# Kernel optimization log

Measured on AMD Instinct MI355X. Metric: run time of the kernel, lower is better.

Reference implementation:

```python
import jax, jax.numpy as jnp
import numpy as np

DIM = 1024
HEADS = 16
HEAD_DIM = DIM // HEADS


def setup_inputs() -> dict:
    key = jax.random.key(0)
    ks = jax.random.split(key, 12)
    B, Tq, Tk = 2, 2048, 2048
    inp = {
        "query": jax.random.normal(ks[0], (B, Tq, DIM), jnp.float32),
        "key": jax.random.normal(ks[1], (B, Tk, DIM), jnp.float32),
        "value": jax.random.normal(ks[2], (B, Tk, DIM), jnp.float32),
        "mask": jax.random.randint(ks[3], (B, 1, Tq, Tk), 0, 2, jnp.int32),
        # xavier-uniform projection weights (stored [out,in] like torch), zero biases
        "wq": jax.random.uniform(ks[4], (DIM, DIM), jnp.float32, -1.0, 1.0) * np.sqrt(6.0 / (2 * DIM)),
        "wk": jax.random.uniform(ks[5], (DIM, DIM), jnp.float32, -1.0, 1.0) * np.sqrt(6.0 / (2 * DIM)),
        "wv": jax.random.uniform(ks[6], (DIM, DIM), jnp.float32, -1.0, 1.0) * np.sqrt(6.0 / (2 * DIM)),
        "wo": jax.random.uniform(ks[7], (DIM, DIM), jnp.float32, -1.0, 1.0) * np.sqrt(6.0 / (2 * DIM)),
        "bq": jnp.zeros((DIM,), jnp.float32),
        "bk": jnp.zeros((DIM,), jnp.float32),
        "bv": jnp.zeros((DIM,), jnp.float32),
        "bo": jnp.zeros((DIM,), jnp.float32),
    }
    return inp


def reference(query, key, value, mask, wq, wk, wv, wo, bq, bk, bv, bo):
    B, Tq, C = query.shape
    Tk = key.shape[1]
    scale = 1.0 / np.sqrt(HEAD_DIM)
    # projections (torch Linear: x @ W.T + b) -> [B, H, T, Dh]
    q = (query @ wq.T + bq).reshape(B, Tq, HEADS, HEAD_DIM).transpose(0, 2, 1, 3)
    k = (key @ wk.T + bk).reshape(B, Tk, HEADS, HEAD_DIM).transpose(0, 2, 1, 3)
    v = (value @ wv.T + bv).reshape(B, Tk, HEADS, HEAD_DIM).transpose(0, 2, 1, 3)
    scores = jnp.einsum("bhqd,bhkd->bhqk", q, k) * scale
    scores = jnp.clip(scores, -100.0, 100.0)
    scores = jnp.where(mask == 0, -jnp.inf, scores)
    attn = jax.nn.softmax(scores, axis=-1)  # dropout is identity in eval
    out = jnp.einsum("bhqk,bhkd->bhqd", attn, v)
    out = out.transpose(0, 2, 1, 3).reshape(B, Tq, HEADS * HEAD_DIM)
    return out @ wo.T + bo
```

## Files before the change

### kernel.cpp

```cpp
#include <hip/hip_runtime.h>
#include <hip/hip_bf16.h>
#include <stdint.h>


typedef __bf16 bf16;
typedef __bf16 bf16x4 __attribute__((ext_vector_type(4)));
typedef __bf16 bf16x8 __attribute__((ext_vector_type(8)));
typedef float f32x4 __attribute__((ext_vector_type(4)));

#define MFMA_BF16(a, b, c) __builtin_amdgcn_mfma_f32_16x16x32_bf16((a), (b), (c), 0, 0, 0)
#define NEG_INF (-__builtin_inff())

__device__ __forceinline__ void async_load16(const void* g, void* l) {
  __builtin_amdgcn_global_load_lds((const __attribute__((address_space(1))) void*)g,
                                   (__attribute__((address_space(3))) void*)l, 16, 0, 0);
}

__global__ __launch_bounds__(256) void cvt_f32_bf16(
    const float* __restrict__ s0, const float* __restrict__ s1, const float* __restrict__ s2,
    const float* __restrict__ s3, const float* __restrict__ s4, const float* __restrict__ s5,
    const float* __restrict__ s6,
    bf16* __restrict__ d0, bf16* __restrict__ d1, bf16* __restrict__ d2,
    bf16* __restrict__ d3, bf16* __restrict__ d4, bf16* __restrict__ d5,
    bf16* __restrict__ d6) {
  const int z = blockIdx.y;
  const float* s = (z == 0) ? s0 : (z == 1) ? s1 : (z == 2) ? s2 : (z == 3) ? s3
                   : (z == 4) ? s4 : (z == 5) ? s5 : s6;
  bf16* d = (z == 0) ? d0 : (z == 1) ? d1 : (z == 2) ? d2 : (z == 3) ? d3
            : (z == 4) ? d4 : (z == 5) ? d5 : d6;
  const int n4 = (z < 3) ? (4 * 1024 * 1024 / 4) : (1024 * 1024 / 4);
  const int stride = gridDim.x * 256;
  for (int i = blockIdx.x * 256 + threadIdx.x; i < n4; i += stride) {
    const float4 v = ((const float4*)s)[i];
    bf16x4 o;
    o[0] = (bf16)v.x; o[1] = (bf16)v.y; o[2] = (bf16)v.z; o[3] = (bf16)v.w;
    ((bf16x4*)d)[i] = o;
  }
}

__global__ __launch_bounds__(256) void pack_mask_kernel(const int* __restrict__ mask,
                                                        unsigned long long* __restrict__ bits) {
  const int t = blockIdx.x * 256 + threadIdx.x;
  const int v = mask[t];
  const unsigned long long b = __ballot(v != 0);
  if ((threadIdx.x & 63) == 0) bits[t >> 6] = b;
}

__global__ __launch_bounds__(256) void gemm_bt_bias(
    const bf16* __restrict__ X0, const bf16* __restrict__ X1, const bf16* __restrict__ X2,
    const bf16* __restrict__ W0, const bf16* __restrict__ W1, const bf16* __restrict__ W2,
    const float* __restrict__ Bi0, const float* __restrict__ Bi1, const float* __restrict__ Bi2,
    bf16* __restrict__ O0, bf16* __restrict__ O1, bf16* __restrict__ O2,
    float* __restrict__ OF, int K, int N, int vz, int f32out) {
  const int z = blockIdx.z;
  const bf16* X   = (z == 0) ? X0  : (z == 1) ? X1  : X2;
  const bf16* W   = (z == 0) ? W0  : (z == 1) ? W1  : W2;
  const float* Bi = (z == 0) ? Bi0 : (z == 1) ? Bi1 : Bi2;
  bf16* O         = (z == 0) ? O0  : (z == 1) ? O1  : O2;

  __shared__ __align__(16) unsigned char smem_raw[34816];
  bf16* As  = (bf16*)smem_raw;
  bf16* Bs  = As + 128 * 64;
  bf16* Tt  = (bf16*)smem_raw;
  float* Tf = (float*)smem_raw;

  const int tid = threadIdx.x;
  const int lane = tid & 63;
  const int w = tid >> 6;
  const int la = lane & 15;
  const int qa = lane >> 4;
  const int m0 = blockIdx.x * 128;
  const int n0 = blockIdx.y * 128;
  const int wm = (w & 1) * 64;
  const int wn = (w >> 1) * 64;

  f32x4 acc[4][4];
  for (int i = 0; i < 4; ++i)
    for (int j = 0; j < 4; ++j) acc[i][j] = (f32x4){0.f, 0.f, 0.f, 0.f};

  for (int k0 = 0; k0 < K; k0 += 64) {
    for (int i = 0; i < 4; ++i) {
      const int cb = i * 256 + w * 64;
      const int c = cb + lane;
      const int row = c >> 3;
      const int cc = (c & 7) * 8;
      async_load16(X + (size_t)(m0 + row) * K + k0 + cc, As + (size_t)cb * 8);
      async_load16(W + (size_t)(n0 + row) * K + k0 + cc, Bs + (size_t)cb * 8);
    }
    __syncthreads();
    for (int kk = 0; kk < 64; kk += 32) {
      bf16x8 af[4], bfr[4];
      for (int mt = 0; mt < 4; ++mt)
        af[mt] = *(const bf16x8*)&As[(wm + mt * 16 + la) * 64 + kk + qa * 8];
      for (int nt = 0; nt < 4; ++nt)
        bfr[nt] = *(const bf16x8*)&Bs[(wn + nt * 16 + la) * 64 + kk + qa * 8];
      for (int mt = 0; mt < 4; ++mt)
        for (int nt = 0; nt < 4; ++nt)
          acc[mt][nt] = MFMA_BF16(af[mt], bfr[nt], acc[mt][nt]);
    }
    __syncthreads();
  }

  if (f32out) {
    for (int pass = 0; pass < 2; ++pass) {
      if ((w & 1) == pass) {
        for (int mt = 0; mt < 4; ++mt)
          for (int nt = 0; nt < 4; ++nt)
            for (int r = 0; r < 4; ++r) {
              const int rl = mt * 16 + qa * 4 + r;
              const int cl = wn + nt * 16 + la;
              Tf[rl * 132 + cl] = acc[mt][nt][r] + Bi[n0 + cl];
            }
      }
      __syncthreads();
      for (int i = 0; i < 8; ++i) {
        const int rl = i * 8 + (tid >> 5);
        const int cl = (tid & 31) * 4;
        const float4 vv = *(const float4*)&Tf[rl * 132 + cl];
        *(float4*)&OF[(size_t)(m0 + pass * 64 + rl) * N + n0 + cl] = vv;
      }
      __syncthreads();
    }
  } else if (z != vz) {
    for (int mt = 0; mt < 4; ++mt)
      for (int nt = 0; nt < 4; ++nt)
        for (int r = 0; r < 4; ++r) {
          const int rl = wm + mt * 16 + qa * 4 + r;
          const int cl = wn + nt * 16 + la;
          Tt[rl * 136 + cl] = (bf16)(acc[mt][nt][r] + Bi[n0 + cl]);
        }
    __syncthreads();
    for (int i = 0; i < 8; ++i) {
      const int rl = i * 16 + (tid >> 4);
      const int cc = (tid & 15) * 8;
      *(bf16x8*)&O[(size_t)(m0 + rl) * N + n0 + cc] = *(const bf16x8*)&Tt[rl * 136 + cc];
    }
  } else {
    for (int mt = 0; mt < 4; ++mt)
      for (int nt = 0; nt < 4; ++nt)
        for (int r = 0; r < 4; ++r) {
          const int rl = wm + mt * 16 + qa * 4 + r;
          const int cl = wn + nt * 16 + la;
          Tt[cl * 136 + rl] = (bf16)(acc[mt][nt][r] + Bi[n0 + cl]);
        }
    __syncthreads();
    const int bb = m0 >> 11;
    const int k0t = m0 & 2047;
    for (int i = 0; i < 8; ++i) {
      const int cl = i * 16 + (tid >> 4);
      const int rr = (tid & 15) * 8;
      *(bf16x8*)&O[((size_t)(bb * 1024 + n0 + cl)) * 2048 + k0t + rr] =
          *(const bf16x8*)&Tt[cl * 136 + rr];
    }
  }
}

__global__ __launch_bounds__(256, 3) void attn_kernel(
    const bf16* __restrict__ Qp, const bf16* __restrict__ Kp, const bf16* __restrict__ Vt,
    const unsigned long long* __restrict__ mbits, bf16* __restrict__ AO) {
  __shared__ bf16 Kb[2][64 * 64];
  __shared__ bf16 Vb[2][64 * 64];

  const int tid = threadIdx.x;
  const int lane = tid & 63;
  const int w = tid >> 6;
  const int la = lane & 15;
  const int qa = lane >> 4;
  const int la7 = la & 7;
  const int b = blockIdx.y >> 4;
  const int h = blockIdx.y & 15;
  const int q0 = blockIdx.x * 64 + w * 16;

  const float SCALE = 0.18033688011112042f;

  const size_t kbase = (size_t)(b * 2048) * 1024 + h * 64;
  const size_t vbase = ((size_t)(b * 16 + h) * 64) * 2048;
  const unsigned long long* mrow = mbits + ((size_t)(b * 2048 + q0 + la)) * 32;

  const int cb0 = w * 64;
  const int cb1 = 256 + w * 64;
  const int c0 = cb0 + lane, c1 = cb1 + lane;
  const int r0 = c0 >> 3, j0 = (c0 & 7) ^ (r0 & 7);
  const int r1 = c1 >> 3, j1 = (c1 & 7) ^ (r1 & 7);
  const bf16* kp0 = Kp + kbase + (size_t)r0 * 1024 + j0 * 8;
  const bf16* kp1 = Kp + kbase + (size_t)r1 * 1024 + j1 * 8;
  const bf16* vp0 = Vt + vbase + (size_t)r0 * 2048 + j0 * 8;
  const bf16* vp1 = Vt + vbase + (size_t)r1 * 2048 + j1 * 8;

  bf16x8 qf[2];
  for (int kk = 0; kk < 2; ++kk)
    qf[kk] = *(const bf16x8*)&Qp[(size_t)(b * 2048 + q0 + la) * 1024 + h * 64 + kk * 32 + qa * 8];

  bf16x8 ones;
  for (int j = 0; j < 8; ++j) ones[j] = (bf16)1.0f;

  f32x4 oacc[5];
  for (int d = 0; d < 5; ++d) oacc[d] = (f32x4){0.f, 0.f, 0.f, 0.f};

  async_load16(kp0, &Kb[0][cb0 * 8]);
  async_load16(kp1, &Kb[0][cb1 * 8]);
  async_load16(vp0, &Vb[0][cb0 * 8]);
  async_load16(vp1, &Vb[0][cb1 * 8]);
  __syncthreads();

  const int srcA = ((qa & 1) << 5) + la;
  const int srcB = srcA + 16;
  const bool hi = (qa >= 2);

  for (int kt = 0; kt < 32; ++kt) {
    const int p = kt & 1;
    const bf16* Kc = Kb[p];
    const bf16* Vc = Vb[p];

    if (kt < 31) {
      bf16* Kn = Kb[p ^ 1];
      bf16* Vn = Vb[p ^ 1];
      kp0 += 64 * 1024; kp1 += 64 * 1024;
      vp0 += 64;        vp1 += 64;
      async_load16(kp0, &Kn[cb0 * 8]);
      async_load16(kp1, &Kn[cb1 * 8]);
      async_load16(vp0, &Vn[cb0 * 8]);
      async_load16(vp1, &Vn[cb1 * 8]);
    }

    const unsigned long long mv = mrow[kt];

    f32x4 s[4];
    for (int nt = 0; nt < 4; ++nt) s[nt] = (f32x4){0.f, 0.f, 0.f, 0.f};
#pragma unroll
    for (int kk = 0; kk < 2; ++kk)
#pragma unroll
      for (int nt = 0; nt < 4; ++nt) {
        const bf16x8 kf = *(const bf16x8*)&Kc[(nt * 16 + la) * 64 + (((kk * 4 + qa) ^ la7) * 8)];
        s[nt] = MFMA_BF16(kf, qf[kk], s[nt]);
      }

    uint32_t pk[4][2];
#pragma unroll
    for (int nt = 0; nt < 4; ++nt) {
      const unsigned mbitsw = (unsigned)(mv >> (nt * 16 + qa * 4));
      bf16x4 t4;
      for (int r = 0; r < 4; ++r) {
        const float bitf = (float)((mbitsw >> r) & 1u);
        t4[r] = (bf16)(bitf * exp2f(s[nt][r] * SCALE));
      }
      const uint32_t* u = (const uint32_t*)&t4;
      pk[nt][0] = u[0];
      pk[nt][1] = u[1];
    }

#pragma unroll
    for (int ks = 0; ks < 2; ++ks) {
      const uint32_t a0x = __shfl((int)pk[2 * ks][0], srcA);
      const uint32_t a1x = __shfl((int)pk[2 * ks + 1][0], srcA);
      const uint32_t a0y = __shfl((int)pk[2 * ks][1], srcA);
      const uint32_t a1y = __shfl((int)pk[2 * ks + 1][1], srcA);
      const uint32_t b0x = __shfl((int)pk[2 * ks][0], srcB);
      const uint32_t b1x = __shfl((int)pk[2 * ks + 1][0], srcB);
      const uint32_t b0y = __shfl((int)pk[2 * ks][1], srcB);
      const uint32_t b1y = __shfl((int)pk[2 * ks + 1][1], srcB);
      uint32_t pfu[4];
      pfu[0] = hi ? a1x : a0x;
      pfu[1] = hi ? a1y : a0y;
      pfu[2] = hi ? b1x : b0x;
      pfu[3] = hi ? b1y : b0y;
      const bf16x8 pf = *(const bf16x8*)pfu;
#pragma unroll
      for (int dt = 0; dt < 4; ++dt) {
        const bf16x8 vf = *(const bf16x8*)&Vc[(dt * 16 + la) * 64 + (((ks * 4 + qa) ^ la7) * 8)];
        oacc[dt] = MFMA_BF16(vf, pf, oacc[dt]);
      }
      oacc[4] = MFMA_BF16(ones, pf, oacc[4]);
    }

    __syncthreads();
  }

  const float rl = 1.0f / oacc[4][0];
  for (int dt = 0; dt < 4; ++dt) {
    bf16x4 o4;
    for (int r = 0; r < 4; ++r) o4[r] = (bf16)(oacc[dt][r] * rl);
    *(bf16x4*)&AO[(size_t)(b * 2048 + q0 + la) * 1024 + h * 64 + dt * 16 + qa * 4] = o4;
  }
}

extern "C" void kernel_launch(void* const* d_in, const int* in_sizes, int n_in,
                              void* d_out, int out_size, void* d_ws, size_t ws_size,
                              hipStream_t stream) {
  const float* q    = (const float*)d_in[0];
  const float* k    = (const float*)d_in[1];
  const float* v    = (const float*)d_in[2];
  const int*   mask = (const int*)d_in[3];
  const float* wq   = (const float*)d_in[4];
  const float* wk   = (const float*)d_in[5];
  const float* wv   = (const float*)d_in[6];
  const float* wo   = (const float*)d_in[7];
  const float* bq   = (const float*)d_in[8];
  const float* bk   = (const float*)d_in[9];
  const float* bv   = (const float*)d_in[10];
  const float* bo   = (const float*)d_in[11];

  const size_t M4 = (size_t)4 * 1024 * 1024, M1 = (size_t)1024 * 1024;
  bf16* qb  = (bf16*)d_ws;
  bf16* kb  = qb + M4;
  bf16* vb  = kb + M4;
  bf16* wqb = vb + M4;
  bf16* wkb = wqb + M1;
  bf16* wvb = wkb + M1;
  bf16* wob = wvb + M1;
  bf16* Qp  = wob + M1;
  bf16* Kp  = Qp + M4;
  bf16* Vt  = Kp + M4;
  unsigned long long* mb = (unsigned long long*)(Vt + M4);
  bf16* AO  = qb;
  float* out = (float*)d_out;

  cvt_f32_bf16<<<dim3(2048, 7), dim3(256), 0, stream>>>(
      q, k, v, wq, wk, wv, wo, qb, kb, vb, wqb, wkb, wvb, wob);
  pack_mask_kernel<<<dim3(8388608 / 256), dim3(256), 0, stream>>>(mask, mb);
  gemm_bt_bias<<<dim3(32, 8, 3), dim3(256), 0, stream>>>(
      qb, kb, vb, wqb, wkb, wvb, bq, bk, bv, Qp, Kp, Vt, nullptr, 1024, 1024, 2, 0);
  attn_kernel<<<dim3(32, 32), dim3(256), 0, stream>>>(Qp, Kp, Vt, mb, AO);
  gemm_bt_bias<<<dim3(32, 8, 1), dim3(256), 0, stream>>>(
      AO, AO, AO, wob, wob, wob, bo, bo, bo, nullptr, nullptr, nullptr, out, 1024, 1024, -1, 1);
}
```

Before: 306.7 us.

## Fold softmax scale into Q projection and drop lane shuffles in PV MFMA

The softmax scale (with its log2e factor) is now applied in the Q projection epilogue, so the attention loop skips a multiply per score. The P·V product switches to 16x16x16 bf16 MFMAs whose operand layout matches the score accumulator layout. This removes the eight cross-lane shuffles and selects per block and reads V as 4-element fragments instead. The next mask word is also prefetched one iteration ahead. The trade is twice as many MFMA issues for PV and the row sum, plus more register pressure from holding all the V fragments.

```diff
diff --git a/kernel.cpp b/kernel.cpp
--- a/kernel.cpp
+++ b/kernel.cpp
@@ -7,9 +7,14 @@
 typedef __bf16 bf16x4 __attribute__((ext_vector_type(4)));
 typedef __bf16 bf16x8 __attribute__((ext_vector_type(8)));
 typedef float f32x4 __attribute__((ext_vector_type(4)));
+typedef short s16x4 __attribute__((ext_vector_type(4)));
 
 #define MFMA_BF16(a, b, c) __builtin_amdgcn_mfma_f32_16x16x32_bf16((a), (b), (c), 0, 0, 0)
-#define NEG_INF (-__builtin_inff())
+
+__device__ __forceinline__ f32x4 mfma16(bf16x4 a, bf16x4 b, f32x4 c) {
+  return __builtin_amdgcn_mfma_f32_16x16x16bf16_1k(
+      __builtin_bit_cast(s16x4, a), __builtin_bit_cast(s16x4, b), c, 0, 0, 0);
+}
 
 __device__ __forceinline__ void async_load16(const void* g, void* l) {
   __builtin_amdgcn_global_load_lds((const __attribute__((address_space(1))) void*)g,
@@ -51,7 +56,7 @@
     const bf16* __restrict__ W0, const bf16* __restrict__ W1, const bf16* __restrict__ W2,
     const float* __restrict__ Bi0, const float* __restrict__ Bi1, const float* __restrict__ Bi2,
     bf16* __restrict__ O0, bf16* __restrict__ O1, bf16* __restrict__ O2,
-    float* __restrict__ OF, int K, int N, int vz, int f32out) {
+    float* __restrict__ OF, int K, int N, int vz, int f32out, float qs) {
   const int z = blockIdx.z;
   const bf16* X   = (z == 0) ? X0  : (z == 1) ? X1  : X2;
   const bf16* W   = (z == 0) ? W0  : (z == 1) ? W1  : W2;
@@ -122,12 +127,13 @@
       __syncthreads();
     }
   } else if (z != vz) {
+    const float sc = (z == 0) ? qs : 1.0f;
     for (int mt = 0; mt < 4; ++mt)
       for (int nt = 0; nt < 4; ++nt)
         for (int r = 0; r < 4; ++r) {
           const int rl = wm + mt * 16 + qa * 4 + r;
           const int cl = wn + nt * 16 + la;
-          Tt[rl * 136 + cl] = (bf16)(acc[mt][nt][r] + Bi[n0 + cl]);
+          Tt[rl * 136 + cl] = (bf16)((acc[mt][nt][r] + Bi[n0 + cl]) * sc);
         }
     __syncthreads();
     for (int i = 0; i < 8; ++i) {
@@ -171,8 +177,6 @@
   const int h = blockIdx.y & 15;
   const int q0 = blockIdx.x * 64 + w * 16;
 
-  const float SCALE = 0.18033688011112042f;
-
   const size_t kbase = (size_t)(b * 2048) * 1024 + h * 64;
   const size_t vbase = ((size_t)(b * 16 + h) * 64) * 2048;
   const unsigned long long* mrow = mbits + ((size_t)(b * 2048 + q0 + la)) * 32;
@@ -191,8 +195,13 @@
   for (int kk = 0; kk < 2; ++kk)
     qf[kk] = *(const bf16x8*)&Qp[(size_t)(b * 2048 + q0 + la) * 1024 + h * 64 + kk * 32 + qa * 8];
 
-  bf16x8 ones;
-  for (int j = 0; j < 8; ++j) ones[j] = (bf16)1.0f;
+  bf16x4 ones4;
+  for (int j = 0; j < 4; ++j) ones4[j] = (bf16)1.0f;
+
+  int cofs[4];
+#pragma unroll
+  for (int nt = 0; nt < 4; ++nt)
+    cofs[nt] = (((nt * 2 + (qa >> 1)) ^ la7) * 8) + ((qa & 1) * 4);
 
   f32x4 oacc[5];
   for (int d = 0; d < 5; ++d) oacc[d] = (f32x4){0.f, 0.f, 0.f, 0.f};
@@ -201,17 +210,15 @@
   async_load16(kp1, &Kb[0][cb1 * 8]);
   async_load16(vp0, &Vb[0][cb0 * 8]);
   async_load16(vp1, &Vb[0][cb1 * 8]);
+  unsigned long long mv = mrow[0];
   __syncthreads();
-
-  const int srcA = ((qa & 1) << 5) + la;
-  const int srcB = srcA + 16;
-  const bool hi = (qa >= 2);
 
   for (int kt = 0; kt < 32; ++kt) {
     const int p = kt & 1;
     const bf16* Kc = Kb[p];
     const bf16* Vc = Vb[p];
 
+    unsigned long long mvn = 0;
     if (kt < 31) {
       bf16* Kn = Kb[p ^ 1];
       bf16* Vn = Vb[p ^ 1];
@@ -221,9 +228,8 @@
       async_load16(kp1, &Kn[cb1 * 8]);
       async_load16(vp0, &Vn[cb0 * 8]);
       async_load16(vp1, &Vn[cb1 * 8]);
-    }
-
-    const unsigned long long mv = mrow[kt];
+      mvn = mrow[kt + 1];
+    }
 
     f32x4 s[4];
     for (int nt = 0; nt < 4; ++nt) s[nt] = (f32x4){0.f, 0.f, 0.f, 0.f};
@@ -235,44 +241,35 @@
         s[nt] = MFMA_BF16(kf, qf[kk], s[nt]);
       }
 
-    uint32_t pk[4][2];
+    bf16x4 vf[4][4];
+#pragma unroll
+    for (int dt = 0; dt < 4; ++dt)
+#pragma unroll
+      for (int nt = 0; nt < 4; ++nt)
+        vf[dt][nt] = *(const bf16x4*)&Vc[(dt * 16 + la) * 64 + cofs[nt]];
+
+    const unsigned long long mvs = mv >> (qa * 4);
+    const uint32_t mlo = (uint32_t)mvs, mhi = (uint32_t)(mvs >> 32);
+    bf16x4 pfr[4];
 #pragma unroll
     for (int nt = 0; nt < 4; ++nt) {
-      const unsigned mbitsw = (unsigned)(mv >> (nt * 16 + qa * 4));
-      bf16x4 t4;
+      const uint32_t mw = ((nt & 2) ? mhi : mlo) >> ((nt & 1) * 16);
+#pragma unroll
       for (int r = 0; r < 4; ++r) {
-        const float bitf = (float)((mbitsw >> r) & 1u);
-        t4[r] = (bf16)(bitf * exp2f(s[nt][r] * SCALE));
+        const float bitf = (float)((mw >> r) & 1u);
+        pfr[nt][r] = (bf16)(bitf * exp2f(s[nt][r]));
       }
-      const uint32_t* u = (const uint32_t*)&t4;
-      pk[nt][0] = u[0];
-      pk[nt][1] = u[1];
-    }
-
-#pragma unroll
-    for (int ks = 0; ks < 2; ++ks) {
-      const uint32_t a0x = __shfl((int)pk[2 * ks][0], srcA);
-      const uint32_t a1x = __shfl((int)pk[2 * ks + 1][0], srcA);
-      const uint32_t a0y = __shfl((int)pk[2 * ks][1], srcA);
-      const uint32_t a1y = __shfl((int)pk[2 * ks + 1][1], srcA);
-      const uint32_t b0x = __shfl((int)pk[2 * ks][0], srcB);
-      const uint32_t b1x = __shfl((int)pk[2 * ks + 1][0], srcB);
-      const uint32_t b0y = __shfl((int)pk[2 * ks][1], srcB);
-      const uint32_t b1y = __shfl((int)pk[2 * ks + 1][1], srcB);
-      uint32_t pfu[4];
-      pfu[0] = hi ? a1x : a0x;
-      pfu[1] = hi ? a1y : a0y;
-      pfu[2] = hi ? b1x : b0x;
-      pfu[3] = hi ? b1y : b0y;
-      const bf16x8 pf = *(const bf16x8*)pfu;
-#pragma unroll
-      for (int dt = 0; dt < 4; ++dt) {
-        const bf16x8 vf = *(const bf16x8*)&Vc[(dt * 16 + la) * 64 + (((ks * 4 + qa) ^ la7) * 8)];
-        oacc[dt] = MFMA_BF16(vf, pf, oacc[dt]);
-      }
-      oacc[4] = MFMA_BF16(ones, pf, oacc[4]);
-    }
-
+    }
+
+#pragma unroll
+    for (int nt = 0; nt < 4; ++nt) {
+#pragma unroll
+      for (int dt = 0; dt < 4; ++dt)
+        oacc[dt] = mfma16(vf[dt][nt], pfr[nt], oacc[dt]);
+      oacc[4] = mfma16(ones4, pfr[nt], oacc[4]);
+    }
+
+    mv = mvn;
     __syncthreads();
   }
 
@@ -315,12 +312,14 @@
   bf16* AO  = qb;
   float* out = (float*)d_out;
 
+  const float QSCALE = 0.18033688011112042f;
+
   cvt_f32_bf16<<<dim3(2048, 7), dim3(256), 0, stream>>>(
       q, k, v, wq, wk, wv, wo, qb, kb, vb, wqb, wkb, wvb, wob);
   pack_mask_kernel<<<dim3(8388608 / 256), dim3(256), 0, stream>>>(mask, mb);
   gemm_bt_bias<<<dim3(32, 8, 3), dim3(256), 0, stream>>>(
-      qb, kb, vb, wqb, wkb, wvb, bq, bk, bv, Qp, Kp, Vt, nullptr, 1024, 1024, 2, 0);
+      qb, kb, vb, wqb, wkb, wvb, bq, bk, bv, Qp, Kp, Vt, nullptr, 1024, 1024, 2, 0, QSCALE);
   attn_kernel<<<dim3(32, 32), dim3(256), 0, stream>>>(Qp, Kp, Vt, mb, AO);
   gemm_bt_bias<<<dim3(32, 8, 1), dim3(256), 0, stream>>>(
-      AO, AO, AO, wob, wob, wob, bo, bo, bo, nullptr, nullptr, nullptr, out, 1024, 1024, -1, 1);
-}
+      AO, AO, AO, wob, wob, wob, bo, bo, bo, nullptr, nullptr, nullptr, out, 1024, 1024, -1, 1, 1.0f);
+}
```

Measured after the change: 300.9 us. About the same (-1.9%).
